# Kernel tuning notes

Measured on AMD Instinct MI355X. Metric: run time of the kernel, lower is better.

Reference implementation:

```python
import jax, jax.numpy as jnp
import numpy as np

N = 50000
E = 1600000
VOCAB = 1000
EMB = 128
HID = 128
OUT = 128


def setup_inputs() -> dict:
    key = jax.random.key(0)
    ks = jax.random.split(key, 8)
    labels = jax.random.randint(ks[0], (N,), 0, VOCAB)
    edge_index = jax.random.randint(ks[1], (2, E), 0, N)
    weight = jax.random.uniform(ks[2], (E,), dtype=jnp.float32)
    emb_table = jax.random.normal(ks[3], (VOCAB, EMB), dtype=jnp.float32) * 0.02
    W1 = jax.random.normal(ks[4], (EMB, HID), dtype=jnp.float32) * (1.0 / np.sqrt(EMB))
    b1 = jnp.zeros((HID,), dtype=jnp.float32)
    W2 = jax.random.normal(ks[5], (HID, OUT), dtype=jnp.float32) * (1.0 / np.sqrt(HID))
    b2 = jnp.zeros((OUT,), dtype=jnp.float32)
    return {"labels": labels, "edge_index": edge_index, "weight": weight,
            "emb_table": emb_table, "W1": W1, "b1": b1, "W2": W2, "b2": b2}


def _gcn_conv(x, src, dst, ew, W, b, n_nodes):
    # PyG GCNConv: linear transform, then symmetric-normalized weighted aggregation.
    x = x @ W  # [N, F_out]
    deg = jax.ops.segment_sum(ew, dst, num_segments=n_nodes)  # weighted in-degree (incl. self loops)
    dinv = jnp.where(deg > 0, jax.lax.rsqrt(deg), 0.0)
    norm = dinv[src] * ew * dinv[dst]  # [E_tot]
    msg = x[src] * norm[:, None]  # gather + scale
    out = jax.ops.segment_sum(msg, dst, num_segments=n_nodes)  # scatter-add
    return out + b


def reference(labels, edge_index, weight, emb_table, W1, b1, W2, b2):
    n_nodes = emb_table.shape[0] if False else labels.shape[0]
    # add self loops with weight 1.0 (GCNConv default add_self_loops=True)
    loop = jnp.arange(n_nodes, dtype=edge_index.dtype)
    src = jnp.concatenate([edge_index[0], loop])
    dst = jnp.concatenate([edge_index[1], loop])
    ew = jnp.concatenate([weight.astype(jnp.float32), jnp.ones((n_nodes,), jnp.float32)])

    x = emb_table[labels]  # embedding lookup [N, EMB]
    x = _gcn_conv(x, src, dst, ew, W1, b1, n_nodes)
    x = jax.nn.relu(x)
    x = _gcn_conv(x, src, dst, ew, W2, b2, n_nodes)
    return x
```

## Files before the change

### kernel.cpp

```cpp
#include <hip/hip_runtime.h>
#include <hip/hip_fp16.h>


#define CHUNKS 256
#define BSTAGE 2816

typedef float floatx2 __attribute__((ext_vector_type(2)));

__global__ __launch_bounds__(1024) void hist_temb_kernel(
    const int* __restrict__ dst, int* __restrict__ hist, int e, int chunk,
    int nb, int bact, const float* __restrict__ emb,
    const float* __restrict__ W1, unsigned* __restrict__ temb8, int vocab) {
  __shared__ unsigned lh[1024];
  __shared__ float xs[32][128];
  int b = blockIdx.x, t = threadIdx.x;
  if (b < bact) {
    lh[t] = 0;
    __syncthreads();
    int start = b * chunk, end = min(e, start + chunk);
    for (int i = start + t; i < end; i += 1024) atomicAdd(&lh[dst[i] >> 6], 1u);
    __syncthreads();
    if (t < nb) hist[(size_t)t * CHUNKS + b] = (int)lh[t];
  } else {
    int row = t >> 5, fl = t & 31;
    int r = (b - bact) * 32 + row;
    if (r < vocab)
      *(float4*)&xs[row][fl * 4] = *(const float4*)(emb + (size_t)r * 128 + fl * 4);
    __syncthreads();
    if (r < vocab) {
      float a0 = 0.f, a1 = 0.f, a2 = 0.f, a3 = 0.f;
#pragma unroll 4
      for (int k = 0; k < 128; ++k) {
        float xv = xs[row][k];
        float4 w4 = *(const float4*)(W1 + k * 128 + fl * 4);
        a0 = fmaf(xv, w4.x, a0); a1 = fmaf(xv, w4.y, a1);
        a2 = fmaf(xv, w4.z, a2); a3 = fmaf(xv, w4.w, a3);
      }
      int pk = __builtin_amdgcn_cvt_pk_fp8_f32(a0 * 64.f, a1 * 64.f, 0, false);
      pk = __builtin_amdgcn_cvt_pk_fp8_f32(a2 * 64.f, a3 * 64.f, pk, true);
      temb8[(size_t)r * 32 + fl] = (unsigned)pk;
    }
  }
}

__global__ __launch_bounds__(256) void tembn_kernel(const int* __restrict__ labels,
                                                    const unsigned* __restrict__ temb8,
                                                    unsigned* __restrict__ tembN,
                                                    int n) {
  int i = blockIdx.x * 256 + threadIdx.x;
  int row = i >> 5, fl = i & 31;
  if (row < n) tembN[i] = temb8[(size_t)labels[row] * 32 + fl];
}

__global__ __launch_bounds__(256) void colscan_kernel(const int* __restrict__ hist,
                                                      int* __restrict__ off,
                                                      int* __restrict__ tot,
                                                      int nb, int bact) {
  int k = (blockIdx.x * 256 + threadIdx.x) >> 6;
  int lane = threadIdx.x & 63;
  if (k >= nb) return;
  int carry = 0;
  for (int r = 0; r < CHUNKS / 64; ++r) {
    int b = r * 64 + lane;
    int h = (b < bact) ? hist[(size_t)k * CHUNKS + b] : 0;
    int x = h;
#pragma unroll
    for (int d = 1; d < 64; d <<= 1) {
      int tt = __shfl_up(x, d, 64);
      if (lane >= d) x += tt;
    }
    if (b < bact) off[(size_t)k * CHUNKS + b] = carry + x - h;
    carry += __shfl(x, 63, 64);
  }
  if (lane == 0) tot[k] = carry;
}

__global__ __launch_bounds__(1024) void ebase_kernel(const int* __restrict__ tot,
                                                     int* __restrict__ ebase, int nb) {
  __shared__ int wsum[16];
  int t = threadIdx.x, lane = t & 63, wv = t >> 6;
  int v = (t < nb) ? tot[t] : 0;
  int x = v;
#pragma unroll
  for (int d = 1; d < 64; d <<= 1) {
    int tt = __shfl_up(x, d, 64);
    if (lane >= d) x += tt;
  }
  if (lane == 63) wsum[wv] = x;
  __syncthreads();
  int o = 0;
#pragma unroll
  for (int w = 0; w < 16; ++w) o += (w < wv) ? wsum[w] : 0;
  int excl = x - v + o;
  if (t < nb) ebase[t] = excl;
  if (t == nb - 1) ebase[nb] = excl + v;
}

__global__ __launch_bounds__(1024) void scatter_kernel(
    const int* __restrict__ src, const int* __restrict__ dst,
    const float* __restrict__ w, const int* __restrict__ off,
    const int* __restrict__ ebase, int2* __restrict__ brec, int e, int chunk,
    int nb) {
  __shared__ unsigned bincnt[1024];
  __shared__ int gbase[1024];
  int b = blockIdx.x, t = threadIdx.x;
  bincnt[t] = 0;
  if (t < nb) gbase[t] = ebase[t] + off[(size_t)t * CHUNKS + b];
  __syncthreads();
  int start = b * chunk, end = min(e, start + chunk);
  int s[7], d[7], ps[7];
  float wv[7];
#pragma unroll
  for (int u = 0; u < 7; ++u) {
    int i = start + u * 1024 + t;
    bool ok = i < end;
    s[u] = ok ? src[i] : 0;
    d[u] = ok ? dst[i] : 0;
    wv[u] = ok ? w[i] : 0.f;
  }
#pragma unroll
  for (int u = 0; u < 7; ++u) ps[u] = gbase[d[u] >> 6];
#pragma unroll
  for (int u = 0; u < 7; ++u) {
    int i = start + u * 1024 + t;
    if (i < end) {
      int k = d[u] >> 6;
      unsigned lr = atomicAdd(&bincnt[k], 1u);
      unsigned rx = (unsigned)s[u] | ((unsigned)(d[u] & 63) << 16);
      brec[ps[u] + (int)lr] = make_int2((int)rx, __float_as_int(wv[u]));
    }
  }
}

__global__ __launch_bounds__(256) void bsort_kernel(const int2* __restrict__ brec,
                                                    const int* __restrict__ ebase,
                                                    unsigned* __restrict__ csrE,
                                                    int* __restrict__ rs,
                                                    float* __restrict__ dinv, int n) {
  __shared__ int2 stage[BSTAGE];
  __shared__ unsigned h64[2][64];
  __shared__ unsigned cur[2][64];
  __shared__ float rsum[2][64];
  int k = blockIdx.x, t = threadIdx.x;
  int p = t >> 7;
  int e0 = ebase[k], e1 = ebase[k + 1], cnt = e1 - e0;
  if (t < 128) { h64[t >> 6][t & 63] = 0; rsum[t >> 6][t & 63] = 0.f; }
  __syncthreads();
  bool fits = (cnt <= BSTAGE);
  for (int i = t; i < cnt; i += 256) {
    int2 r = brec[e0 + i];
    if (fits) stage[i] = r;
    unsigned dl = ((unsigned)r.x >> 16) & 63u;
    atomicAdd(&h64[p][dl], 1u);
    atomicAdd(&rsum[p][dl], __int_as_float(r.y));
  }
  __syncthreads();
  if (t < 64) {
    int h0 = (int)h64[0][t];
    int hv = h0 + (int)h64[1][t];
    int x = hv;
#pragma unroll
    for (int d = 1; d < 64; d <<= 1) {
      int tt = __shfl_up(x, d, 64);
      if (t >= d) x += tt;
    }
    int ex = x - hv;
    cur[0][t] = (unsigned)(e0 + ex);
    cur[1][t] = (unsigned)(e0 + ex + h0);
    int v = k * 64 + t;
    if (v <= n) rs[v] = e0 + ex;
    if (v < n) dinv[v] = rsqrtf(1.0f + rsum[0][t] + rsum[1][t]);
  }
  __syncthreads();
  for (int i = t; i < cnt; i += 256) {
    int2 r = fits ? stage[i] : brec[e0 + i];
    unsigned rx = (unsigned)r.x;
    int dl = (int)((rx >> 16) & 63u);
    int pos = (int)atomicAdd(&cur[p][dl], 1u);
    unsigned hb =
        (unsigned)__half_as_ushort(__float2half_rn(__int_as_float(r.y)));
    csrE[pos] = ((rx & 0xffffu) << 16) | hb;
  }
}

__global__ __launch_bounds__(256) void agg1_kernel(
    const int* __restrict__ rs, const unsigned* __restrict__ csrE,
    const float* __restrict__ dinv, const unsigned* __restrict__ tembN,
    const float* __restrict__ b1, unsigned* __restrict__ out8, int n) {
  int wid = (blockIdx.x * blockDim.x + threadIdx.x) >> 6;
  int lane = threadIdx.x & 63;
  if (wid >= n) return;
  int half = lane >> 5, fl = lane & 31;
  unsigned flo = (unsigned)(fl << 2);
  const char* tb = (const char*)tembN;
  float di = dinv[wid];
  float acc0, acc1, acc2, acc3;
  {
    unsigned r8 = *(const unsigned*)(tb + (((unsigned)wid) << 7) + flo);
    floatx2 a = __builtin_amdgcn_cvt_pk_f32_fp8((int)r8, false);
    floatx2 b = __builtin_amdgcn_cvt_pk_f32_fp8((int)r8, true);
    float ss = half ? 0.f : di;
    acc0 = a[0] * ss; acc1 = a[1] * ss; acc2 = b[0] * ss; acc3 = b[1] * ss;
  }
  int base0 = rs[wid], r1v = rs[wid + 1];
  unsigned x = 0;
  if (base0 + lane < r1v) {
    unsigned rec = csrE[base0 + lane];
    float wp = __half2float(__ushort_as_half((unsigned short)(rec & 0xffffu))) *
               dinv[rec >> 16];
    x = (rec & 0xffff0000u) |
        (unsigned)__half_as_ushort(__float2half_rn(wp));
  }
  for (int base = base0; base < r1v; base += 64) {
    unsigned nx = 0;
    if (base + 64 + lane < r1v) {
      unsigned rec = csrE[base + 64 + lane];
      float wp = __half2float(__ushort_as_half((unsigned short)(rec & 0xffffu))) *
                 dinv[rec >> 16];
      nx = (rec & 0xffff0000u) |
           (unsigned)__half_as_ushort(__float2half_rn(wp));
    }
    int nb = min(64, r1v - base);
    int j = 0;
    for (; j + 16 <= nb; j += 16) {
#pragma unroll
      for (int u = 0; u < 8; ++u) {
        unsigned xj = (unsigned)__shfl((int)x, j + 2 * u + half, 64);
        float vj = __half2float(__ushort_as_half((unsigned short)(xj & 0xffffu)));
        unsigned r8 = *(const unsigned*)(tb + ((xj >> 16) << 7) + flo);
        floatx2 a = __builtin_amdgcn_cvt_pk_f32_fp8((int)r8, false);
        floatx2 b = __builtin_amdgcn_cvt_pk_f32_fp8((int)r8, true);
        acc0 = fmaf(a[0], vj, acc0); acc1 = fmaf(a[1], vj, acc1);
        acc2 = fmaf(b[0], vj, acc2); acc3 = fmaf(b[1], vj, acc3);
      }
    }
    for (; j + 2 <= nb; j += 2) {
      unsigned xj = (unsigned)__shfl((int)x, j + half, 64);
      float vj = __half2float(__ushort_as_half((unsigned short)(xj & 0xffffu)));
      unsigned r8 = *(const unsigned*)(tb + ((xj >> 16) << 7) + flo);
      floatx2 a = __builtin_amdgcn_cvt_pk_f32_fp8((int)r8, false);
      floatx2 b = __builtin_amdgcn_cvt_pk_f32_fp8((int)r8, true);
      acc0 = fmaf(a[0], vj, acc0); acc1 = fmaf(a[1], vj, acc1);
      acc2 = fmaf(b[0], vj, acc2); acc3 = fmaf(b[1], vj, acc3);
    }
    if (j < nb) {
      unsigned xj = (unsigned)__shfl((int)x, j, 64);
      float vj0 = __half2float(__ushort_as_half((unsigned short)(xj & 0xffffu)));
      float vj = half ? 0.f : vj0;
      unsigned r8 = *(const unsigned*)(tb + ((xj >> 16) << 7) + flo);
      floatx2 a = __builtin_amdgcn_cvt_pk_f32_fp8((int)r8, false);
      floatx2 b = __builtin_amdgcn_cvt_pk_f32_fp8((int)r8, true);
      acc0 = fmaf(a[0], vj, acc0); acc1 = fmaf(a[1], vj, acc1);
      acc2 = fmaf(b[0], vj, acc2); acc3 = fmaf(b[1], vj, acc3);
    }
    x = nx;
  }
  acc0 += __shfl_xor(acc0, 32, 64);
  acc1 += __shfl_xor(acc1, 32, 64);
  acc2 += __shfl_xor(acc2, 32, 64);
  acc3 += __shfl_xor(acc3, 32, 64);
  if (half == 0) {
    float4 b4 = ((const float4*)b1)[fl];
    acc0 = fmaxf(fmaf(acc0, di, b4.x * 64.f), 0.f);
    acc1 = fmaxf(fmaf(acc1, di, b4.y * 64.f), 0.f);
    acc2 = fmaxf(fmaf(acc2, di, b4.z * 64.f), 0.f);
    acc3 = fmaxf(fmaf(acc3, di, b4.w * 64.f), 0.f);
    int pk = __builtin_amdgcn_cvt_pk_fp8_f32(acc0, acc1, 0, false);
    pk = __builtin_amdgcn_cvt_pk_fp8_f32(acc2, acc3, pk, true);
    out8[(size_t)wid * 32 + fl] = (unsigned)pk;
  }
}

__global__ __launch_bounds__(256) void agg2_kernel(
    const int* __restrict__ rs, const unsigned* __restrict__ csrE,
    const float* __restrict__ dinv, const unsigned* __restrict__ h8,
    float* __restrict__ out, int n) {
  int wid = (blockIdx.x * blockDim.x + threadIdx.x) >> 6;
  int lane = threadIdx.x & 63;
  if (wid >= n) return;
  int half = lane >> 5, fl = lane & 31;
  unsigned flo = (unsigned)(fl << 2);
  const char* hb = (const char*)h8;
  float di = dinv[wid];
  float acc0, acc1, acc2, acc3;
  {
    unsigned r8 = *(const unsigned*)(hb + (((unsigned)wid) << 7) + flo);
    floatx2 a = __builtin_amdgcn_cvt_pk_f32_fp8((int)r8, false);
    floatx2 b = __builtin_amdgcn_cvt_pk_f32_fp8((int)r8, true);
    float ss = half ? 0.f : di;
    acc0 = a[0] * ss; acc1 = a[1] * ss; acc2 = b[0] * ss; acc3 = b[1] * ss;
  }
  int base0 = rs[wid], r1v = rs[wid + 1];
  unsigned x = 0;
  if (base0 + lane < r1v) {
    unsigned rec = csrE[base0 + lane];
    float wp = __half2float(__ushort_as_half((unsigned short)(rec & 0xffffu))) *
               dinv[rec >> 16];
    x = (rec & 0xffff0000u) |
        (unsigned)__half_as_ushort(__float2half_rn(wp));
  }
  for (int base = base0; base < r1v; base += 64) {
    unsigned nx = 0;
    if (base + 64 + lane < r1v) {
      unsigned rec = csrE[base + 64 + lane];
      float wp = __half2float(__ushort_as_half((unsigned short)(rec & 0xffffu))) *
                 dinv[rec >> 16];
      nx = (rec & 0xffff0000u) |
           (unsigned)__half_as_ushort(__float2half_rn(wp));
    }
    int nb = min(64, r1v - base);
    int j = 0;
    for (; j + 16 <= nb; j += 16) {
#pragma unroll
      for (int u = 0; u < 8; ++u) {
        unsigned xj = (unsigned)__shfl((int)x, j + 2 * u + half, 64);
        float vj = __half2float(__ushort_as_half((unsigned short)(xj & 0xffffu)));
        unsigned r8 = *(const unsigned*)(hb + ((xj >> 16) << 7) + flo);
        floatx2 a = __builtin_amdgcn_cvt_pk_f32_fp8((int)r8, false);
        floatx2 b = __builtin_amdgcn_cvt_pk_f32_fp8((int)r8, true);
        acc0 = fmaf(a[0], vj, acc0); acc1 = fmaf(a[1], vj, acc1);
        acc2 = fmaf(b[0], vj, acc2); acc3 = fmaf(b[1], vj, acc3);
      }
    }
    for (; j + 2 <= nb; j += 2) {
      unsigned xj = (unsigned)__shfl((int)x, j + half, 64);
      float vj = __half2float(__ushort_as_half((unsigned short)(xj & 0xffffu)));
      unsigned r8 = *(const unsigned*)(hb + ((xj >> 16) << 7) + flo);
      floatx2 a = __builtin_amdgcn_cvt_pk_f32_fp8((int)r8, false);
      floatx2 b = __builtin_amdgcn_cvt_pk_f32_fp8((int)r8, true);
      acc0 = fmaf(a[0], vj, acc0); acc1 = fmaf(a[1], vj, acc1);
      acc2 = fmaf(b[0], vj, acc2); acc3 = fmaf(b[1], vj, acc3);
    }
    if (j < nb) {
      unsigned xj = (unsigned)__shfl((int)x, j, 64);
      float vj0 = __half2float(__ushort_as_half((unsigned short)(xj & 0xffffu)));
      float vj = half ? 0.f : vj0;
      unsigned r8 = *(const unsigned*)(hb + ((xj >> 16) << 7) + flo);
      floatx2 a = __builtin_amdgcn_cvt_pk_f32_fp8((int)r8, false);
      floatx2 b = __builtin_amdgcn_cvt_pk_f32_fp8((int)r8, true);
      acc0 = fmaf(a[0], vj, acc0); acc1 = fmaf(a[1], vj, acc1);
      acc2 = fmaf(b[0], vj, acc2); acc3 = fmaf(b[1], vj, acc3);
    }
    x = nx;
  }
  acc0 += __shfl_xor(acc0, 32, 64);
  acc1 += __shfl_xor(acc1, 32, 64);
  acc2 += __shfl_xor(acc2, 32, 64);
  acc3 += __shfl_xor(acc3, 32, 64);
  if (half == 0) {
    float sc = di * 0.015625f;
    ((float4*)(out + (size_t)wid * 128))[fl] =
        make_float4(acc0 * sc, acc1 * sc, acc2 * sc, acc3 * sc);
  }
}

__global__ __launch_bounds__(256) void gemm_bias_kernel(float* __restrict__ y,
                                                        const float* __restrict__ W,
                                                        const float* __restrict__ bias,
                                                        int n) {
  __shared__ float xs[32][128];
  int tid = threadIdx.x;
  int tc = tid & 31;
  int tr = tid >> 5;
  int rb = blockIdx.x * 32;
  {
    const float4* xg = (const float4*)(y + (size_t)rb * 128);
    float4* xls = (float4*)&xs[0][0];
#pragma unroll
    for (int i = 0; i < 4; ++i) {
      int idx = tid + i * 256;
      int row = rb + (idx >> 5);
      float4 val = (row < n) ? xg[idx] : make_float4(0.f, 0.f, 0.f, 0.f);
      xls[idx] = val;
    }
  }
  __syncthreads();
  int j0 = tc * 4;
  float4 b4 = *(const float4*)(bias + j0);
  float acc[4][4];
#pragma unroll
  for (int r = 0; r < 4; ++r) {
    acc[r][0] = b4.x; acc[r][1] = b4.y; acc[r][2] = b4.z; acc[r][3] = b4.w;
  }
#pragma unroll 4
  for (int k = 0; k < 128; ++k) {
    float4 w4 = *(const float4*)(W + k * 128 + j0);
#pragma unroll
    for (int r = 0; r < 4; ++r) {
      float xv = xs[tr * 4 + r][k];
      acc[r][0] = fmaf(xv, w4.x, acc[r][0]);
      acc[r][1] = fmaf(xv, w4.y, acc[r][1]);
      acc[r][2] = fmaf(xv, w4.z, acc[r][2]);
      acc[r][3] = fmaf(xv, w4.w, acc[r][3]);
    }
  }
#pragma unroll
  for (int r = 0; r < 4; ++r) {
    int row = rb + tr * 4 + r;
    if (row < n)
      *(float4*)(y + (size_t)row * 128 + j0) =
          make_float4(acc[r][0], acc[r][1], acc[r][2], acc[r][3]);
  }
}

extern "C" void kernel_launch(void* const* d_in, const int* in_sizes, int n_in,
                              void* d_out, int out_size, void* d_ws, size_t ws_size,
                              hipStream_t stream) {
  const int* labels = (const int*)d_in[0];
  const int* edge_index = (const int*)d_in[1];
  const float* weight = (const float*)d_in[2];
  const float* emb = (const float*)d_in[3];
  const float* W1 = (const float*)d_in[4];
  const float* b1 = (const float*)d_in[5];
  const float* W2 = (const float*)d_in[6];
  const float* b2 = (const float*)d_in[7];

  int n = in_sizes[0];
  int e = in_sizes[1] / 2;
  int vocab = in_sizes[3] / 128;
  const int* srcp = edge_index;
  const int* dstp = edge_index + e;

  int nb = (n + 63) >> 6;
  int chunk = (e + CHUNKS - 1) / CHUNKS;
  int bact = (e + chunk - 1) / chunk;
  int tblocks = (vocab + 31) / 32;

  float* ws = (float*)d_ws;
  size_t o = 0;
  auto alloc_f = [&](size_t c) { float* p = ws + o; o += (c + 255) & ~(size_t)255; return p; };
  int*      hist  = (int*)alloc_f((size_t)nb * CHUNKS);
  int*      off   = (int*)alloc_f((size_t)nb * CHUNKS);
  int*      tot   = (int*)alloc_f(nb);
  int*      ebase = (int*)alloc_f(nb + 1);
  int2*     brec  = (int2*)alloc_f((size_t)e * 2);
  int*      rs    = (int*)alloc_f(n + 1);
  unsigned* csrE  = (unsigned*)alloc_f(e);
  float*    dinv  = alloc_f(n);
  unsigned* temb8 = (unsigned*)alloc_f((size_t)vocab * 32);
  unsigned* tembN = (unsigned*)alloc_f((size_t)n * 32);
  unsigned* out8  = (unsigned*)alloc_f((size_t)n * 32);
  (void)ws_size;

  dim3 b256(256);
  dim3 b1024(1024);
  int gagg = (int)(((size_t)n * 64 + 255) / 256);

  hist_temb_kernel<<<bact + tblocks, b1024, 0, stream>>>(dstp, hist, e, chunk, nb,
                                                         bact, emb, W1, temb8, vocab);
  tembn_kernel<<<(n * 32 + 255) / 256, b256, 0, stream>>>(labels, temb8, tembN, n);
  colscan_kernel<<<(nb * 64 + 255) / 256, b256, 0, stream>>>(hist, off, tot, nb, bact);
  ebase_kernel<<<1, b1024, 0, stream>>>(tot, ebase, nb);
  scatter_kernel<<<bact, b1024, 0, stream>>>(srcp, dstp, weight, off, ebase, brec,
                                             e, chunk, nb);
  bsort_kernel<<<nb, b256, 0, stream>>>(brec, ebase, csrE, rs, dinv, n);
  agg1_kernel<<<gagg, b256, 0, stream>>>(rs, csrE, dinv, tembN, b1, out8, n);
  agg2_kernel<<<gagg, b256, 0, stream>>>(rs, csrE, dinv, out8, (float*)d_out, n);
  gemm_bias_kernel<<<(n + 31) / 32, b256, 0, stream>>>((float*)d_out, W2, b2, n);
}
```

Measured before the change: 168.3 us.

## Process four edges per wavefront step with 8-byte gathers and packed FMA

Both aggregation kernels now split each 64-lane wavefront into four 16-lane groups instead of two 32-lane halves. Each lane loads 8 fp8 features with one uint2 load and accumulates into float2 vectors with packed multiply-add, so four neighbour rows are gathered per loop step. Lanes past the end of a short batch read row 0 with weight zero, which replaces the old tail-handling loops with one unroll-4 loop. The final reduction adds one more shuffle level across the four groups, and the output writes become wider per lane.

After: 183.4 us. 1.09x slower.

```diff
diff --git a/kernel.cpp b/kernel.cpp
--- a/kernel.cpp
+++ b/kernel.cpp
@@ -6,6 +6,7 @@
 #define BSTAGE 2816
 
 typedef float floatx2 __attribute__((ext_vector_type(2)));
+__device__ __forceinline__ floatx2 splat2(float v) { return (floatx2){v, v}; }
 
 __global__ __launch_bounds__(1024) void hist_temb_kernel(
     const int* __restrict__ dst, int* __restrict__ hist, int e, int chunk,
@@ -183,6 +184,7 @@
   }
 }
 
+
 __global__ __launch_bounds__(256) void agg1_kernel(
     const int* __restrict__ rs, const unsigned* __restrict__ csrE,
     const float* __restrict__ dinv, const unsigned* __restrict__ tembN,
@@ -190,17 +192,18 @@
   int wid = (blockIdx.x * blockDim.x + threadIdx.x) >> 6;
   int lane = threadIdx.x & 63;
   if (wid >= n) return;
-  int half = lane >> 5, fl = lane & 31;
-  unsigned flo = (unsigned)(fl << 2);
-  const char* tb = (const char*)tembN;
+  int q = lane >> 4, fl = lane & 15;
+  const char* tbp = (const char*)tembN + (fl << 3);
   float di = dinv[wid];
-  float acc0, acc1, acc2, acc3;
-  {
-    unsigned r8 = *(const unsigned*)(tb + (((unsigned)wid) << 7) + flo);
-    floatx2 a = __builtin_amdgcn_cvt_pk_f32_fp8((int)r8, false);
-    floatx2 b = __builtin_amdgcn_cvt_pk_f32_fp8((int)r8, true);
-    float ss = half ? 0.f : di;
-    acc0 = a[0] * ss; acc1 = a[1] * ss; acc2 = b[0] * ss; acc3 = b[1] * ss;
+  floatx2 acc0 = {0.f, 0.f}, acc1 = {0.f, 0.f}, acc2 = {0.f, 0.f},
+          acc3 = {0.f, 0.f};
+  if (q == 0) {
+    uint2 r8 = *(const uint2*)(tbp + (((unsigned)wid) << 7));
+    floatx2 d2 = splat2(di);
+    acc0 = __builtin_amdgcn_cvt_pk_f32_fp8((int)r8.x, false) * d2;
+    acc1 = __builtin_amdgcn_cvt_pk_f32_fp8((int)r8.x, true) * d2;
+    acc2 = __builtin_amdgcn_cvt_pk_f32_fp8((int)r8.y, false) * d2;
+    acc3 = __builtin_amdgcn_cvt_pk_f32_fp8((int)r8.y, true) * d2;
   }
   int base0 = rs[wid], r1v = rs[wid + 1];
   unsigned x = 0;
@@ -208,8 +211,7 @@
     unsigned rec = csrE[base0 + lane];
     float wp = __half2float(__ushort_as_half((unsigned short)(rec & 0xffffu))) *
                dinv[rec >> 16];
-    x = (rec & 0xffff0000u) |
-        (unsigned)__half_as_ushort(__float2half_rn(wp));
+    x = (rec & 0xffff0000u) | (unsigned)__half_as_ushort(__float2half_rn(wp));
   }
   for (int base = base0; base < r1v; base += 64) {
     unsigned nx = 0;
@@ -217,57 +219,46 @@
       unsigned rec = csrE[base + 64 + lane];
       float wp = __half2float(__ushort_as_half((unsigned short)(rec & 0xffffu))) *
                  dinv[rec >> 16];
-      nx = (rec & 0xffff0000u) |
-           (unsigned)__half_as_ushort(__float2half_rn(wp));
+      nx = (rec & 0xffff0000u) | (unsigned)__half_as_ushort(__float2half_rn(wp));
     }
     int nb = min(64, r1v - base);
-    int j = 0;
-    for (; j + 16 <= nb; j += 16) {
-#pragma unroll
-      for (int u = 0; u < 8; ++u) {
-        unsigned xj = (unsigned)__shfl((int)x, j + 2 * u + half, 64);
-        float vj = __half2float(__ushort_as_half((unsigned short)(xj & 0xffffu)));
-        unsigned r8 = *(const unsigned*)(tb + ((xj >> 16) << 7) + flo);
-        floatx2 a = __builtin_amdgcn_cvt_pk_f32_fp8((int)r8, false);
-        floatx2 b = __builtin_amdgcn_cvt_pk_f32_fp8((int)r8, true);
-        acc0 = fmaf(a[0], vj, acc0); acc1 = fmaf(a[1], vj, acc1);
-        acc2 = fmaf(b[0], vj, acc2); acc3 = fmaf(b[1], vj, acc3);
-      }
-    }
-    for (; j + 2 <= nb; j += 2) {
-      unsigned xj = (unsigned)__shfl((int)x, j + half, 64);
+#pragma unroll 4
+    for (int j = 0; j < nb; j += 4) {
+      unsigned xj = (unsigned)__shfl((int)x, j + q, 64);
       float vj = __half2float(__ushort_as_half((unsigned short)(xj & 0xffffu)));
-      unsigned r8 = *(const unsigned*)(tb + ((xj >> 16) << 7) + flo);
-      floatx2 a = __builtin_amdgcn_cvt_pk_f32_fp8((int)r8, false);
-      floatx2 b = __builtin_amdgcn_cvt_pk_f32_fp8((int)r8, true);
-      acc0 = fmaf(a[0], vj, acc0); acc1 = fmaf(a[1], vj, acc1);
-      acc2 = fmaf(b[0], vj, acc2); acc3 = fmaf(b[1], vj, acc3);
-    }
-    if (j < nb) {
-      unsigned xj = (unsigned)__shfl((int)x, j, 64);
-      float vj0 = __half2float(__ushort_as_half((unsigned short)(xj & 0xffffu)));
-      float vj = half ? 0.f : vj0;
-      unsigned r8 = *(const unsigned*)(tb + ((xj >> 16) << 7) + flo);
-      floatx2 a = __builtin_amdgcn_cvt_pk_f32_fp8((int)r8, false);
-      floatx2 b = __builtin_amdgcn_cvt_pk_f32_fp8((int)r8, true);
-      acc0 = fmaf(a[0], vj, acc0); acc1 = fmaf(a[1], vj, acc1);
-      acc2 = fmaf(b[0], vj, acc2); acc3 = fmaf(b[1], vj, acc3);
+      floatx2 v2 = splat2(vj);
+      uint2 r8 = *(const uint2*)(tbp + ((xj >> 16) << 7));
+      acc0 += __builtin_amdgcn_cvt_pk_f32_fp8((int)r8.x, false) * v2;
+      acc1 += __builtin_amdgcn_cvt_pk_f32_fp8((int)r8.x, true) * v2;
+      acc2 += __builtin_amdgcn_cvt_pk_f32_fp8((int)r8.y, false) * v2;
+      acc3 += __builtin_amdgcn_cvt_pk_f32_fp8((int)r8.y, true) * v2;
     }
     x = nx;
   }
-  acc0 += __shfl_xor(acc0, 32, 64);
-  acc1 += __shfl_xor(acc1, 32, 64);
-  acc2 += __shfl_xor(acc2, 32, 64);
-  acc3 += __shfl_xor(acc3, 32, 64);
-  if (half == 0) {
-    float4 b4 = ((const float4*)b1)[fl];
-    acc0 = fmaxf(fmaf(acc0, di, b4.x * 64.f), 0.f);
-    acc1 = fmaxf(fmaf(acc1, di, b4.y * 64.f), 0.f);
-    acc2 = fmaxf(fmaf(acc2, di, b4.z * 64.f), 0.f);
-    acc3 = fmaxf(fmaf(acc3, di, b4.w * 64.f), 0.f);
-    int pk = __builtin_amdgcn_cvt_pk_fp8_f32(acc0, acc1, 0, false);
-    pk = __builtin_amdgcn_cvt_pk_fp8_f32(acc2, acc3, pk, true);
-    out8[(size_t)wid * 32 + fl] = (unsigned)pk;
+#pragma unroll
+  for (int d = 16; d < 64; d <<= 1) {
+    acc0[0] += __shfl_xor(acc0[0], d, 64); acc0[1] += __shfl_xor(acc0[1], d, 64);
+    acc1[0] += __shfl_xor(acc1[0], d, 64); acc1[1] += __shfl_xor(acc1[1], d, 64);
+    acc2[0] += __shfl_xor(acc2[0], d, 64); acc2[1] += __shfl_xor(acc2[1], d, 64);
+    acc3[0] += __shfl_xor(acc3[0], d, 64); acc3[1] += __shfl_xor(acc3[1], d, 64);
+  }
+  if (q == 0) {
+    float4 bA = ((const float4*)b1)[fl * 2];
+    float4 bB = ((const float4*)b1)[fl * 2 + 1];
+    float o0 = fmaxf(fmaf(acc0[0], di, bA.x * 64.f), 0.f);
+    float o1 = fmaxf(fmaf(acc0[1], di, bA.y * 64.f), 0.f);
+    float o2 = fmaxf(fmaf(acc1[0], di, bA.z * 64.f), 0.f);
+    float o3 = fmaxf(fmaf(acc1[1], di, bA.w * 64.f), 0.f);
+    float o4 = fmaxf(fmaf(acc2[0], di, bB.x * 64.f), 0.f);
+    float o5 = fmaxf(fmaf(acc2[1], di, bB.y * 64.f), 0.f);
+    float o6 = fmaxf(fmaf(acc3[0], di, bB.z * 64.f), 0.f);
+    float o7 = fmaxf(fmaf(acc3[1], di, bB.w * 64.f), 0.f);
+    int pk0 = __builtin_amdgcn_cvt_pk_fp8_f32(o0, o1, 0, false);
+    pk0 = __builtin_amdgcn_cvt_pk_fp8_f32(o2, o3, pk0, true);
+    int pk1 = __builtin_amdgcn_cvt_pk_fp8_f32(o4, o5, 0, false);
+    pk1 = __builtin_amdgcn_cvt_pk_fp8_f32(o6, o7, pk1, true);
+    *(uint2*)(out8 + (size_t)wid * 32 + fl * 2) =
+        make_uint2((unsigned)pk0, (unsigned)pk1);
   }
 }
 
@@ -278,17 +269,18 @@
   int wid = (blockIdx.x * blockDim.x + threadIdx.x) >> 6;
   int lane = threadIdx.x & 63;
   if (wid >= n) return;
-  int half = lane >> 5, fl = lane & 31;
-  unsigned flo = (unsigned)(fl << 2);
-  const char* hb = (const char*)h8;
+  int q = lane >> 4, fl = lane & 15;
+  const char* hbp = (const char*)h8 + (fl << 3);
   float di = dinv[wid];
-  float acc0, acc1, acc2, acc3;
-  {
-    unsigned r8 = *(const unsigned*)(hb + (((unsigned)wid) << 7) + flo);
-    floatx2 a = __builtin_amdgcn_cvt_pk_f32_fp8((int)r8, false);
-    floatx2 b = __builtin_amdgcn_cvt_pk_f32_fp8((int)r8, true);
-    float ss = half ? 0.f : di;
-    acc0 = a[0] * ss; acc1 = a[1] * ss; acc2 = b[0] * ss; acc3 = b[1] * ss;
+  floatx2 acc0 = {0.f, 0.f}, acc1 = {0.f, 0.f}, acc2 = {0.f, 0.f},
+          acc3 = {0.f, 0.f};
+  if (q == 0) {
+    uint2 r8 = *(const uint2*)(hbp + (((unsigned)wid) << 7));
+    floatx2 d2 = splat2(di);
+    acc0 = __builtin_amdgcn_cvt_pk_f32_fp8((int)r8.x, false) * d2;
+    acc1 = __builtin_amdgcn_cvt_pk_f32_fp8((int)r8.x, true) * d2;
+    acc2 = __builtin_amdgcn_cvt_pk_f32_fp8((int)r8.y, false) * d2;
+    acc3 = __builtin_amdgcn_cvt_pk_f32_fp8((int)r8.y, true) * d2;
   }
   int base0 = rs[wid], r1v = rs[wid + 1];
   unsigned x = 0;
@@ -296,8 +288,7 @@
     unsigned rec = csrE[base0 + lane];
     float wp = __half2float(__ushort_as_half((unsigned short)(rec & 0xffffu))) *
                dinv[rec >> 16];
-    x = (rec & 0xffff0000u) |
-        (unsigned)__half_as_ushort(__float2half_rn(wp));
+    x = (rec & 0xffff0000u) | (unsigned)__half_as_ushort(__float2half_rn(wp));
   }
   for (int base = base0; base < r1v; base += 64) {
     unsigned nx = 0;
@@ -305,52 +296,36 @@
       unsigned rec = csrE[base + 64 + lane];
       float wp = __half2float(__ushort_as_half((unsigned short)(rec & 0xffffu))) *
                  dinv[rec >> 16];
-      nx = (rec & 0xffff0000u) |
-           (unsigned)__half_as_ushort(__float2half_rn(wp));
+      nx = (rec & 0xffff0000u) | (unsigned)__half_as_ushort(__float2half_rn(wp));
     }
     int nb = min(64, r1v - base);
-    int j = 0;
-    for (; j + 16 <= nb; j += 16) {
-#pragma unroll
-      for (int u = 0; u < 8; ++u) {
-        unsigned xj = (unsigned)__shfl((int)x, j + 2 * u + half, 64);
-        float vj = __half2float(__ushort_as_half((unsigned short)(xj & 0xffffu)));
-        unsigned r8 = *(const unsigned*)(hb + ((xj >> 16) << 7) + flo);
-        floatx2 a = __builtin_amdgcn_cvt_pk_f32_fp8((int)r8, false);
-        floatx2 b = __builtin_amdgcn_cvt_pk_f32_fp8((int)r8, true);
-        acc0 = fmaf(a[0], vj, acc0); acc1 = fmaf(a[1], vj, acc1);
-        acc2 = fmaf(b[0], vj, acc2); acc3 = fmaf(b[1], vj, acc3);
-      }
-    }
-    for (; j + 2 <= nb; j += 2) {
-      unsigned xj = (unsigned)__shfl((int)x, j + half, 64);
+#pragma unroll 4
+    for (int j = 0; j < nb; j += 4) {
+      unsigned xj = (unsigned)__shfl((int)x, j + q, 64);
       float vj = __half2float(__ushort_as_half((unsigned short)(xj & 0xffffu)));
-      unsigned r8 = *(const unsigned*)(hb + ((xj >> 16) << 7) + flo);
-      floatx2 a = __builtin_amdgcn_cvt_pk_f32_fp8((int)r8, false);
-      floatx2 b = __builtin_amdgcn_cvt_pk_f32_fp8((int)r8, true);
-      acc0 = fmaf(a[0], vj, acc0); acc1 = fmaf(a[1], vj, acc1);
-      acc2 = fmaf(b[0], vj, acc2); acc3 = fmaf(b[1], vj, acc3);
-    }
-    if (j < nb) {
-      unsigned xj = (unsigned)__shfl((int)x, j, 64);
-      float vj0 = __half2float(__ushort_as_half((unsigned short)(xj & 0xffffu)));
-      float vj = half ? 0.f : vj0;
-      unsigned r8 = *(const unsigned*)(hb + ((xj >> 16) << 7) + flo);
-      floatx2 a = __builtin_amdgcn_cvt_pk_f32_fp8((int)r8, false);
-      floatx2 b = __builtin_amdgcn_cvt_pk_f32_fp8((int)r8, true);
-      acc0 = fmaf(a[0], vj, acc0); acc1 = fmaf(a[1], vj, acc1);
-      acc2 = fmaf(b[0], vj, acc2); acc3 = fmaf(b[1], vj, acc3);
+      floatx2 v2 = splat2(vj);
+      uint2 r8 = *(const uint2*)(hbp + ((xj >> 16) << 7));
+      acc0 += __builtin_amdgcn_cvt_pk_f32_fp8((int)r8.x, false) * v2;
+      acc1 += __builtin_amdgcn_cvt_pk_f32_fp8((int)r8.x, true) * v2;
+      acc2 += __builtin_amdgcn_cvt_pk_f32_fp8((int)r8.y, false) * v2;
+      acc3 += __builtin_amdgcn_cvt_pk_f32_fp8((int)r8.y, true) * v2;
     }
     x = nx;
   }
-  acc0 += __shfl_xor(acc0, 32, 64);
-  acc1 += __shfl_xor(acc1, 32, 64);
-  acc2 += __shfl_xor(acc2, 32, 64);
-  acc3 += __shfl_xor(acc3, 32, 64);
-  if (half == 0) {
+#pragma unroll
+  for (int d = 16; d < 64; d <<= 1) {
+    acc0[0] += __shfl_xor(acc0[0], d, 64); acc0[1] += __shfl_xor(acc0[1], d, 64);
+    acc1[0] += __shfl_xor(acc1[0], d, 64); acc1[1] += __shfl_xor(acc1[1], d, 64);
+    acc2[0] += __shfl_xor(acc2[0], d, 64); acc2[1] += __shfl_xor(acc2[1], d, 64);
+    acc3[0] += __shfl_xor(acc3[0], d, 64); acc3[1] += __shfl_xor(acc3[1], d, 64);
+  }
+  if (q == 0) {
     float sc = di * 0.015625f;
-    ((float4*)(out + (size_t)wid * 128))[fl] =
-        make_float4(acc0 * sc, acc1 * sc, acc2 * sc, acc3 * sc);
+    float* rowp = out + (size_t)wid * 128 + fl * 8;
+    *(float4*)rowp = make_float4(acc0[0] * sc, acc0[1] * sc, acc1[0] * sc,
+                                 acc1[1] * sc);
+    *(float4*)(rowp + 4) = make_float4(acc2[0] * sc, acc2[1] * sc,
+                                       acc3[0] * sc, acc3[1] * sc);
   }
 }
 
```
